# Kernel tuning notes

Measured on AMD Instinct MI355X. Metric: run time of the kernel, lower is better.

The kernel has to match this reference:

```python
import jax, jax.numpy as jnp
import numpy as np
from jax.scipy.linalg import cho_solve

N, D, T, K, P = 4000, 256, 52, 20, 100
EPS = 1e-8


def _make_kernel(length_scale):
    # RBF kernel over time grid with the same jitter-doubling rule as the torch code.
    t = np.arange(T, dtype=np.float32)
    sq = (t[None, :] - t[:, None]) ** 2
    Kmat = np.exp(-0.5 * sq / np.float32(length_scale) ** 2).astype(np.float32)
    jitter = 1e-4
    eye = np.eye(T, dtype=np.float32)
    while True:
        if np.linalg.cond(Kmat + jitter * eye) < 1e4:
            break
        jitter *= 2
        if jitter > 0.1:
            break
    return jnp.asarray(Kmat + jitter * eye)

K_LAMBDA = _make_kernel(T / 4)  # lambda GP kernel, shared across all k
K_PHI = _make_kernel(T / 3)     # phi GP kernel, shared across all k


def setup_inputs() -> dict:
    key = jax.random.key(0)
    ks = jax.random.split(key, 7)
    lambda_ = jax.random.normal(ks[0], (N, K, T), dtype=jnp.float32)
    phi = jax.random.normal(ks[1], (K, D, T), dtype=jnp.float32)
    gamma = 0.1 * jax.random.normal(ks[2], (P, K), dtype=jnp.float32)
    G = jax.random.normal(ks[3], (N, P), dtype=jnp.float32)
    Y = (jax.random.uniform(ks[4], (N, D, T)) < 0.05).astype(jnp.float32)
    logit_prev_t = jax.random.normal(ks[5], (D, T), dtype=jnp.float32) - 3.0
    event_times = jax.random.randint(ks[6], (N, D), 0, T)
    return dict(lambda_=lambda_, phi=phi, gamma=gamma, G=G, Y=Y,
                logit_prev_t=logit_prev_t, event_times=event_times)


def reference(lambda_, phi, gamma, G, Y, logit_prev_t, event_times):
    # --- forward: softmax over topics, sigmoid disease probs, mixture ---
    theta = jax.nn.softmax(lambda_, axis=1)          # [N,K,T]
    phi_prob = jax.nn.sigmoid(phi)                   # [K,D,T]
    pi = jnp.einsum('nkt,kdt->ndt', theta, phi_prob) # [N,D,T]
    pi = jnp.clip(pi, EPS, 1.0 - EPS)

    # --- survival data loss ---
    tgrid = jnp.arange(T)[None, None, :]             # [1,1,T]
    e = event_times[:, :, None]                      # [N,D,1]
    mask_before = (tgrid < e).astype(pi.dtype)
    mask_at = (tgrid == e).astype(pi.dtype)
    log_pi = jnp.log(pi)
    log_1mpi = jnp.log1p(-pi)
    loss_censored = -jnp.sum(log_1mpi * mask_before)
    loss_event = -jnp.sum(log_pi * mask_at * Y)
    loss_no_event = -jnp.sum(log_1mpi * mask_at * (1.0 - Y))
    data_loss = (loss_censored + loss_event + loss_no_event) / N

    # --- GP prior loss: batched cholesky solves replace per-sample loops ---
    L_lam = jnp.linalg.cholesky(K_LAMBDA)            # [T,T]
    L_phi = jnp.linalg.cholesky(K_PHI)               # [T,T]
    mean_lam = G @ gamma                             # [N,K]
    dev_lam = (lambda_ - mean_lam[:, :, None]).reshape(N * K, T)  # [N*K,T]
    v_lam = cho_solve((L_lam, True), dev_lam.T)      # [T,N*K]
    gp_lambda = 0.5 * jnp.sum(dev_lam.T * v_lam)
    dev_phi = (phi - logit_prev_t[None, :, :]).reshape(K * D, T)  # [K*D,T]
    v_phi = cho_solve((L_phi, True), dev_phi.T)      # [T,K*D]
    gp_phi = 0.5 * jnp.sum(dev_phi.T * v_phi)
    gp_loss = gp_lambda / N + gp_phi / D

    return data_loss + gp_loss
```

## Files before the change

### kernel.cpp

```cpp
#include <hip/hip_runtime.h>
#include <math.h>
#include <string.h>

#define Nn 4000
#define Dd 256
#define Tt 52
#define Kk 20
#define Pp 100
#define TC 13

#define GRID_GRAM 145
#define GRID_DATA 2000
#define GRID_MAIN (GRID_GRAM + GRID_DATA)

#define PB_PHIP 52
#define PB_MEAN 313
#define GRID_PREP (PB_PHIP + PB_MEAN)

#define OFF_W     0
#define OFF_GPART 5408
#define OFF_DLP   5556
#define OFF_CNT   7556
#define OFF_M     7560
#define OFF_PHIP  87560

#define GR_ROWS 64

__global__ __launch_bounds__(256) void prep_kernel(
    const float* __restrict__ phi, const float* __restrict__ gamma,
    const float* __restrict__ G, float* __restrict__ phip_t,
    float* __restrict__ M, unsigned int* __restrict__ cnt) {
    const int bx = blockIdx.x, tid = threadIdx.x;
    if (bx < PB_PHIP) {
        if (bx == 0 && tid == 0) *cnt = 0u;
        int gid = bx * 256 + tid;
        int d = gid / Tt, t = gid - d * Tt;
        float v[Kk];
#pragma unroll
        for (int k = 0; k < Kk; ++k) {
            float x = phi[k * (Dd * Tt) + gid];
            v[k] = 1.f / (1.f + __expf(-x));
        }
#pragma unroll
        for (int k = 0; k < Kk; ++k)
            phip_t[((size_t)t * Kk + k) * Dd + d] = v[k];
        return;
    }
    int gid = (bx - PB_PHIP) * 256 + tid;
    if (gid < Nn * Kk) {
        int n = gid / Kk, k = gid - n * Kk;
        float m = 0.f;
        for (int p = 0; p < Pp; ++p) m += G[n * Pp + p] * gamma[p * Kk + k];
        M[gid] = m;
    }
}

__global__ __launch_bounds__(256, 3) void main_kernel(
    const float* __restrict__ lam, const float* __restrict__ phi,
    const float* __restrict__ logit_prev, const int* __restrict__ ev,
    const float* __restrict__ Y, const float* __restrict__ phip_t,
    const float* __restrict__ M, const float* __restrict__ W,
    float* __restrict__ ws, float* __restrict__ out,
    unsigned int* __restrict__ cnt) {
    __shared__ __align__(16) union SM {
        struct { float thS[TC][8][Kk]; float lamS[8][Kk][TC + 1]; } d;
        struct { float rows[GR_ROWS][56]; } g;
    } sm;
    __shared__ double redd[256];
    __shared__ float wsum[4];
    __shared__ int isLast;
    const int bx = blockIdx.x, tid = threadIdx.x;

    if (bx < GRID_GRAM) {
        const bool isPhi = (bx >= 125);
        const int ntile = isPhi ? 4 : 10;
        const int base = isPhi ? (bx - 125) * 256 : bx * 640;
        const int ta = tid % 13, tb = tid / 13;
        float acc[4][4] = {};
        for (int it = 0; it < ntile; ++it) {
            const int R0 = base + it * GR_ROWS;
            __syncthreads();
            for (int idx = tid; idx < GR_ROWS * Tt; idx += 256) {
                int r = idx / Tt, t = idx - r * Tt;
                int R = R0 + r;
                float v;
                if (isPhi) v = phi[R * Tt + t] - logit_prev[(R & (Dd - 1)) * Tt + t];
                else       v = lam[R * Tt + t] - M[R];
                sm.g.rows[r][t] = v;
            }
            __syncthreads();
            if (tb < 13) {
                for (int r = 0; r < GR_ROWS; ++r) {
                    float4 a = *(const float4*)&sm.g.rows[r][4 * ta];
                    float4 b = *(const float4*)&sm.g.rows[r][4 * tb];
                    float av[4] = {a.x, a.y, a.z, a.w};
                    float bv[4] = {b.x, b.y, b.z, b.w};
#pragma unroll
                    for (int i = 0; i < 4; ++i)
#pragma unroll
                        for (int j = 0; j < 4; ++j) acc[i][j] += av[i] * bv[j];
                }
            }
        }
        double s = 0.0;
        if (tb < 13) {
            const float* Wb = W + (isPhi ? 2704 : 0);
#pragma unroll
            for (int i = 0; i < 4; ++i)
#pragma unroll
                for (int j = 0; j < 4; ++j)
                    s += (double)acc[i][j] *
                         (double)Wb[(4 * ta + i) * Tt + 4 * tb + j];
        }
        redd[tid] = s;
        __syncthreads();
        for (int off = 128; off; off >>= 1) {
            if (tid < off) redd[tid] += redd[tid + off];
            __syncthreads();
        }
        if (tid == 0) {
            ws[OFF_GPART + bx] = (float)redd[0];
            __threadfence();
            unsigned prev = atomicAdd(cnt, 1u);
            isLast = (prev == GRID_MAIN - 1) ? 1 : 0;
        }
    } else {
        const int bid = bx - GRID_GRAM;
        const int d = tid;
        const int ng = bid >> 2;
        const int chunk = bid & 3;
        const int t0 = chunk * TC;
        const int n0 = ng * 8;

        float pvA[Kk], pvB[Kk];
#define LOADPV(BUF, J) do {                                                    \
        const float* pt_ = phip_t + (size_t)(t0 + (J)) * (Kk * Dd) + d;        \
        _Pragma("unroll")                                                      \
        for (int k = 0; k < Kk; ++k) BUF[k] = pt_[k * Dd];                     \
    } while (0)
        LOADPV(pvA, 0);

        int e[8];
#pragma unroll
        for (int g = 0; g < 8; ++g) e[g] = ev[(n0 + g) * Dd + d];

        float Yv[8], acc[8], pie[8], prod[8];
#pragma unroll
        for (int g = 0; g < 8; ++g) {
            acc[g] = 0.f; prod[g] = 1.f; pie[g] = 0.5f; Yv[g] = 0.f;
            if ((unsigned)(e[g] - t0) < (unsigned)TC)
                Yv[g] = __builtin_nontemporal_load(
                    Y + (size_t)((n0 + g) * Dd + d) * Tt + e[g]);
        }

        if (tid < 8 * Kk) {
            int n = tid / Kk, k = tid - n * Kk;
            const float* src = lam + ((size_t)(n0 + n) * Kk + k) * Tt + t0;
#pragma unroll
            for (int j = 0; j < TC; ++j) sm.d.lamS[n][k][j] = src[j];
        }
        __syncthreads();
        if (tid < 8 * TC) {
            int n = tid / TC, j = tid - n * TC;
            float v[Kk];
            float m = -1e30f;
#pragma unroll
            for (int k = 0; k < Kk; ++k) { v[k] = sm.d.lamS[n][k][j]; m = fmaxf(m, v[k]); }
            float s = 0.f;
#pragma unroll
            for (int k = 0; k < Kk; ++k) { v[k] = __expf(v[k] - m); s += v[k]; }
            float inv = 1.f / s;
#pragma unroll
            for (int k = 0; k < Kk; ++k) sm.d.thS[j][n][k] = v[k] * inv;
        }
        __syncthreads();

        float4 c0, c1, c2, c3, c4;
        {
            const float4* thp = (const float4*)&sm.d.thS[0][0][0];
            c0 = thp[0]; c1 = thp[1]; c2 = thp[2]; c3 = thp[3]; c4 = thp[4];
        }

#define COMPUTE(J, PV) do {                                                    \
        const int t_ = t0 + (J);                                               \
        _Pragma("unroll")                                                      \
        for (int g = 0; g < 8; ++g) {                                          \
            float4 n0_, n1_, n2_, n3_, n4_;                                    \
            const bool hasNext = (g < 7) || ((J) < TC - 1);                    \
            if (hasNext) {                                                     \
                const float4* np_ = (g < 7)                                    \
                    ? (const float4*)&sm.d.thS[(J)][g + 1][0]                  \
                    : (const float4*)&sm.d.thS[(J) + 1][0][0];                 \
                n0_ = np_[0]; n1_ = np_[1]; n2_ = np_[2];                      \
                n3_ = np_[3]; n4_ = np_[4];                                    \
            }                                                                  \
            float pi = c0.x*PV[0] + c0.y*PV[1] + c0.z*PV[2] + c0.w*PV[3]       \
                     + c1.x*PV[4] + c1.y*PV[5] + c1.z*PV[6] + c1.w*PV[7]       \
                     + c2.x*PV[8] + c2.y*PV[9] + c2.z*PV[10] + c2.w*PV[11]     \
                     + c3.x*PV[12] + c3.y*PV[13] + c3.z*PV[14] + c3.w*PV[15]   \
                     + c4.x*PV[16] + c4.y*PV[17] + c4.z*PV[18] + c4.w*PV[19];  \
            pi = fminf(fmaxf(pi, 1e-8f), 1.0f - 1e-8f);                        \
            prod[g] *= (t_ <= e[g]) ? (1.f - pi) : 1.f;                        \
            pie[g] = (t_ == e[g]) ? pi : pie[g];                               \
            if (hasNext) { c0 = n0_; c1 = n1_; c2 = n2_; c3 = n3_; c4 = n4_; } \
        }                                                                      \
        if ((((J) & 3) == 3) || ((J) == TC - 1)) {                             \
            _Pragma("unroll")                                                  \
            for (int g = 0; g < 8; ++g) {                                      \
                acc[g] += __logf(prod[g]); prod[g] = 1.f;                      \
            }                                                                  \
        }                                                                      \
    } while (0)

#pragma unroll 1
        for (int j2 = 0; j2 < TC - 1; j2 += 2) {
            LOADPV(pvB, j2 + 1);
            COMPUTE(j2, pvA);
            if (j2 + 2 < TC) LOADPV(pvA, j2 + 2);
            COMPUTE(j2 + 1, pvB);
        }
        COMPUTE(TC - 1, pvA);

        float tsum = 0.f;
#pragma unroll
        for (int g = 0; g < 8; ++g)
            tsum += acc[g] + Yv[g] * (__logf(pie[g]) - __logf(1.f - pie[g]));
        for (int off = 32; off; off >>= 1) tsum += __shfl_down(tsum, off, 64);
        if ((tid & 63) == 0) wsum[tid >> 6] = tsum;
        __syncthreads();
        if (tid == 0) {
            ws[OFF_DLP + bid] = -(wsum[0] + wsum[1] + wsum[2] + wsum[3]);
            __threadfence();
            unsigned prev = atomicAdd(cnt, 1u);
            isLast = (prev == GRID_MAIN - 1) ? 1 : 0;
        }
    }
    __syncthreads();
    if (!isLast) return;

    __threadfence();
    double s = 0.0;
    for (int i = tid; i < GRID_GRAM; i += 256) s += (double)ws[OFF_GPART + i];
    double dl = 0.0;
    for (int i = tid; i < GRID_DATA; i += 256) dl += (double)ws[OFF_DLP + i];
    s += dl / Nn;
    redd[tid] = s;
    __syncthreads();
    for (int off = 128; off; off >>= 1) {
        if (tid < off) redd[tid] += redd[tid + off];
        __syncthreads();
    }
    if (tid == 0) out[0] = (float)redd[0];
}


static void build_K_f(double ls_in, float Kf[52][52]) {
    float ls = (float)ls_in;
    float ls2 = ls * ls;
    for (int i = 0; i < 52; ++i)
        for (int j = 0; j < 52; ++j) {
            float sq = (float)((i - j) * (i - j));
            float arg = (-0.5f * sq) / ls2;
            Kf[i][j] = expf(arg);
        }
}

static void jacobi_eig(double a[52][52], double ev[52]) {
    const int n = 52;
    for (int sweep = 0; sweep < 100; ++sweep) {
        double off = 0;
        for (int p = 0; p < n - 1; ++p)
            for (int q = p + 1; q < n; ++q) off += a[p][q] * a[p][q];
        if (off < 1e-24) break;
        for (int p = 0; p < n - 1; ++p)
            for (int q = p + 1; q < n; ++q) {
                double apq = a[p][q];
                if (fabs(apq) < 1e-300) continue;
                double th = (a[q][q] - a[p][p]) / (2.0 * apq);
                double t = (th >= 0 ? 1.0 : -1.0) / (fabs(th) + sqrt(th * th + 1.0));
                double c = 1.0 / sqrt(t * t + 1.0), s = t * c;
                for (int i = 0; i < n; ++i) {
                    double aip = a[i][p], aiq = a[i][q];
                    a[i][p] = c * aip - s * aiq;
                    a[i][q] = s * aip + c * aiq;
                }
                for (int i = 0; i < n; ++i) {
                    double api = a[p][i], aqi = a[q][i];
                    a[p][i] = c * api - s * aqi;
                    a[q][i] = s * api + c * aqi;
                }
            }
    }
    for (int i = 0; i < n; ++i) ev[i] = a[i][i];
}

static void build_A(const float Kf[52][52], double jitter, double A[52][52]) {
    float jf = (float)jitter;
    for (int i = 0; i < 52; ++i)
        for (int j = 0; j < 52; ++j) A[i][j] = (double)Kf[i][j];
    for (int i = 0; i < 52; ++i) A[i][i] = (double)(float)(Kf[i][i] + jf);
}

static double cond_of(const float Kf[52][52], double jitter) {
    double A[52][52], ev[52];
    build_A(Kf, jitter, A);
    jacobi_eig(A, ev);
    double mx = 0.0, mn = 1e300;
    for (int i = 0; i < 52; ++i) {
        double a = fabs(ev[i]);
        if (a > mx) mx = a;
        if (a < mn) mn = a;
    }
    if (mn <= 0.0) return 1e300;
    return mx / mn;
}

static double find_jitter(const float Kf[52][52]) {
    double jitter = 1e-4;
    while (true) {
        if (cond_of(Kf, jitter) < 1e4) break;
        jitter *= 2.0;
        if (jitter > 0.1) break;
    }
    return jitter;
}

static void chol_inv_scaled(const float Kf[52][52], double jitter, double scale,
                            float* out) {
    const int n = 52;
    double A[52][52], L[52][52];
    build_A(Kf, jitter, A);
    memset(L, 0, sizeof(L));
    for (int j = 0; j < n; ++j) {
        double s = A[j][j];
        for (int k = 0; k < j; ++k) s -= L[j][k] * L[j][k];
        L[j][j] = sqrt(s);
        for (int i = j + 1; i < n; ++i) {
            double v = A[i][j];
            for (int k = 0; k < j; ++k) v -= L[i][k] * L[j][k];
            L[i][j] = v / L[j][j];
        }
    }
    for (int c = 0; c < n; ++c) {
        double y[52], x[52];
        for (int i = 0; i < n; ++i) {
            double v = (i == c) ? 1.0 : 0.0;
            for (int k = 0; k < i; ++k) v -= L[i][k] * y[k];
            y[i] = v / L[i][i];
        }
        for (int i = n - 1; i >= 0; --i) {
            double v = y[i];
            for (int k = i + 1; k < n; ++k) v -= L[k][i] * x[k];
            x[i] = v / L[i][i];
        }
        for (int i = 0; i < n; ++i) out[i * 52 + c] = (float)(x[i] * scale);
    }
}

struct KinvInit {
    float* w;
    KinvInit() {
        if (hipHostMalloc((void**)&w, 5408 * sizeof(float)) != hipSuccess)
            w = (float*)malloc(5408 * sizeof(float));
        float Kf[52][52];
        build_K_f(52.0 / 4.0, Kf);
        chol_inv_scaled(Kf, find_jitter(Kf), 0.5 / Nn, w);
        build_K_f(52.0 / 3.0, Kf);
        chol_inv_scaled(Kf, find_jitter(Kf), 0.5 / Dd, w + 2704);
    }
};
static KinvInit g_kinv;


extern "C" void kernel_launch(void* const* d_in, const int* in_sizes, int n_in,
                              void* d_out, int out_size, void* d_ws, size_t ws_size,
                              hipStream_t stream) {
    (void)in_sizes; (void)n_in; (void)out_size; (void)ws_size;
    const float* lam        = (const float*)d_in[0];
    const float* phi        = (const float*)d_in[1];
    const float* gamma      = (const float*)d_in[2];
    const float* G          = (const float*)d_in[3];
    const float* Y          = (const float*)d_in[4];
    const float* logit_prev = (const float*)d_in[5];
    const int*   ev         = (const int*)d_in[6];
    float* out = (float*)d_out;
    float* ws  = (float*)d_ws;

    hipMemcpyAsync(ws + OFF_W, g_kinv.w, 5408 * sizeof(float),
                   hipMemcpyHostToDevice, stream);

    prep_kernel<<<GRID_PREP, 256, 0, stream>>>(
        phi, gamma, G, ws + OFF_PHIP, ws + OFF_M,
        (unsigned int*)(ws + OFF_CNT));
    main_kernel<<<GRID_MAIN, 256, 0, stream>>>(
        lam, phi, logit_prev, ev, Y, ws + OFF_PHIP, ws + OFF_M, ws + OFF_W,
        ws, out, (unsigned int*)(ws + OFF_CNT));
}
```

Before: 423.1 us.

## Compute softmax directly from global lambda, drop staging buffer and register prefetch

The softmax over topics now reads lambda straight from global memory instead of first staging it in a shared-memory buffer, which removes one barrier and the lamS array. The per-step double-buffered register prefetch of theta is replaced by plain shared-memory loads inside the compute loop. The pi clamp is dropped and the occupancy hint in launch_bounds is removed. This cuts shared memory and register pressure, possibly allowing more resident blocks, at the cost of strided uncoalesced global reads for lambda and exposed LDS latency. Dropping the clamp could let log(1-pi) or log(pi) misbehave when pi reaches 0 or 1.

```diff
diff --git a/kernel.cpp b/kernel.cpp
--- a/kernel.cpp
+++ b/kernel.cpp
@@ -55,7 +55,14 @@
     }
 }
 
-__global__ __launch_bounds__(256, 3) void main_kernel(
+#define PICHAIN(PV)                                                            \
+    (a0.x*PV[0] + a0.y*PV[1] + a0.z*PV[2] + a0.w*PV[3]                         \
+   + a1.x*PV[4] + a1.y*PV[5] + a1.z*PV[6] + a1.w*PV[7]                         \
+   + a2.x*PV[8] + a2.y*PV[9] + a2.z*PV[10] + a2.w*PV[11]                       \
+   + a3.x*PV[12] + a3.y*PV[13] + a3.z*PV[14] + a3.w*PV[15]                     \
+   + a4.x*PV[16] + a4.y*PV[17] + a4.z*PV[18] + a4.w*PV[19])
+
+__global__ __launch_bounds__(256) void main_kernel(
     const float* __restrict__ lam, const float* __restrict__ phi,
     const float* __restrict__ logit_prev, const int* __restrict__ ev,
     const float* __restrict__ Y, const float* __restrict__ phip_t,
@@ -63,8 +70,8 @@
     float* __restrict__ ws, float* __restrict__ out,
     unsigned int* __restrict__ cnt) {
     __shared__ __align__(16) union SM {
-        struct { float thS[TC][8][Kk]; float lamS[8][Kk][TC + 1]; } d;
-        struct { float rows[GR_ROWS][56]; } g;
+        float thS[TC][180];
+        float rows[GR_ROWS][56];
     } sm;
     __shared__ double redd[256];
     __shared__ float wsum[4];
@@ -86,13 +93,13 @@
                 float v;
                 if (isPhi) v = phi[R * Tt + t] - logit_prev[(R & (Dd - 1)) * Tt + t];
                 else       v = lam[R * Tt + t] - M[R];
-                sm.g.rows[r][t] = v;
+                sm.rows[r][t] = v;
             }
             __syncthreads();
             if (tb < 13) {
                 for (int r = 0; r < GR_ROWS; ++r) {
-                    float4 a = *(const float4*)&sm.g.rows[r][4 * ta];
-                    float4 b = *(const float4*)&sm.g.rows[r][4 * tb];
+                    float4 a = *(const float4*)&sm.rows[r][4 * ta];
+                    float4 b = *(const float4*)&sm.rows[r][4 * tb];
                     float av[4] = {a.x, a.y, a.z, a.w};
                     float bv[4] = {b.x, b.y, b.z, b.w};
 #pragma unroll
@@ -132,6 +139,21 @@
         const int t0 = chunk * TC;
         const int n0 = ng * 8;
 
+        if (tid < 8 * TC) {
+            int n = tid / TC, j = tid - n * TC;
+            const float* la = lam + ((size_t)(n0 + n) * Kk) * Tt + t0 + j;
+            float v[Kk];
+            float m = -1e30f;
+#pragma unroll
+            for (int k = 0; k < Kk; ++k) { v[k] = la[k * Tt]; m = fmaxf(m, v[k]); }
+            float s = 0.f;
+#pragma unroll
+            for (int k = 0; k < Kk; ++k) { v[k] = __expf(v[k] - m); s += v[k]; }
+            float inv = 1.f / s;
+#pragma unroll
+            for (int k = 0; k < Kk; ++k) sm.thS[j][n * Kk + k] = v[k] * inv;
+        }
+
         float pvA[Kk], pvB[Kk];
 #define LOADPV(BUF, J) do {                                                    \
         const float* pt_ = phip_t + (size_t)(t0 + (J)) * (Kk * Dd) + d;        \
@@ -152,57 +174,17 @@
                 Yv[g] = __builtin_nontemporal_load(
                     Y + (size_t)((n0 + g) * Dd + d) * Tt + e[g]);
         }
-
-        if (tid < 8 * Kk) {
-            int n = tid / Kk, k = tid - n * Kk;
-            const float* src = lam + ((size_t)(n0 + n) * Kk + k) * Tt + t0;
-#pragma unroll
-            for (int j = 0; j < TC; ++j) sm.d.lamS[n][k][j] = src[j];
-        }
         __syncthreads();
-        if (tid < 8 * TC) {
-            int n = tid / TC, j = tid - n * TC;
-            float v[Kk];
-            float m = -1e30f;
-#pragma unroll
-            for (int k = 0; k < Kk; ++k) { v[k] = sm.d.lamS[n][k][j]; m = fmaxf(m, v[k]); }
-            float s = 0.f;
-#pragma unroll
-            for (int k = 0; k < Kk; ++k) { v[k] = __expf(v[k] - m); s += v[k]; }
-            float inv = 1.f / s;
-#pragma unroll
-            for (int k = 0; k < Kk; ++k) sm.d.thS[j][n][k] = v[k] * inv;
-        }
-        __syncthreads();
-
-        float4 c0, c1, c2, c3, c4;
-        {
-            const float4* thp = (const float4*)&sm.d.thS[0][0][0];
-            c0 = thp[0]; c1 = thp[1]; c2 = thp[2]; c3 = thp[3]; c4 = thp[4];
-        }
 
 #define COMPUTE(J, PV) do {                                                    \
         const int t_ = t0 + (J);                                               \
         _Pragma("unroll")                                                      \
         for (int g = 0; g < 8; ++g) {                                          \
-            float4 n0_, n1_, n2_, n3_, n4_;                                    \
-            const bool hasNext = (g < 7) || ((J) < TC - 1);                    \
-            if (hasNext) {                                                     \
-                const float4* np_ = (g < 7)                                    \
-                    ? (const float4*)&sm.d.thS[(J)][g + 1][0]                  \
-                    : (const float4*)&sm.d.thS[(J) + 1][0][0];                 \
-                n0_ = np_[0]; n1_ = np_[1]; n2_ = np_[2];                      \
-                n3_ = np_[3]; n4_ = np_[4];                                    \
-            }                                                                  \
-            float pi = c0.x*PV[0] + c0.y*PV[1] + c0.z*PV[2] + c0.w*PV[3]       \
-                     + c1.x*PV[4] + c1.y*PV[5] + c1.z*PV[6] + c1.w*PV[7]       \
-                     + c2.x*PV[8] + c2.y*PV[9] + c2.z*PV[10] + c2.w*PV[11]     \
-                     + c3.x*PV[12] + c3.y*PV[13] + c3.z*PV[14] + c3.w*PV[15]   \
-                     + c4.x*PV[16] + c4.y*PV[17] + c4.z*PV[18] + c4.w*PV[19];  \
-            pi = fminf(fmaxf(pi, 1e-8f), 1.0f - 1e-8f);                        \
+            const float4* th = (const float4*)&sm.thS[(J)][g * Kk];   \
+            float4 a0 = th[0], a1 = th[1], a2 = th[2], a3 = th[3], a4 = th[4]; \
+            float pi = PICHAIN(PV);                                            \
             prod[g] *= (t_ <= e[g]) ? (1.f - pi) : 1.f;                        \
             pie[g] = (t_ == e[g]) ? pi : pie[g];                               \
-            if (hasNext) { c0 = n0_; c1 = n1_; c2 = n2_; c3 = n3_; c4 = n4_; } \
         }                                                                      \
         if ((((J) & 3) == 3) || ((J) == TC - 1)) {                             \
             _Pragma("unroll")                                                  \
```

Measured after the change: 440.7 us. 4.1% more time.
